# Performance work log

Measured on AMD Instinct MI355X. Metric: run time of the kernel, lower is better.

The kernel has to match this reference:

```python
import jax, jax.numpy as jnp
import numpy as np

N = 100000
E = 3200000


def setup_inputs() -> dict:
    key = jax.random.key(0)
    ks = jax.random.split(key, 12)
    x = jax.random.normal(ks[0], (N, 124), dtype=jnp.float32)
    pos = jax.random.normal(ks[1], (N, 3), dtype=jnp.float32)
    z = jax.random.normal(ks[2], (N,), dtype=jnp.float32)
    edge_index = jax.random.randint(ks[3], (2, E), 0, N, dtype=jnp.int64)
    def lin(k, fin, fout):
        kw, kb = jax.random.split(k)
        s = 1.0 / np.sqrt(fin)
        W = jax.random.uniform(kw, (fin, fout), minval=-s, maxval=s, dtype=jnp.float32)
        b = jax.random.uniform(kb, (fout,), minval=-s, maxval=s, dtype=jnp.float32)
        return W, b
    W1, b1 = lin(ks[4], 128, 256)
    W2, b2 = lin(ks[5], 256, 256)
    W3, b3 = lin(ks[6], 256, 256)
    W4, b4 = lin(ks[7], 256, 1)
    return {"x": x, "pos": pos, "z": z, "edge_index": edge_index,
            "W1": W1, "b1": b1, "W2": W2, "b2": b2,
            "W3": W3, "b3": b3, "W4": W4, "b4": b4}


def reference(x, pos, z, edge_index, W1, b1, W2, b2, W3, b3, W4, b4):
    # features = hstack(x, pos, z[:, None])  -> [N, input_dim]
    feats = jnp.concatenate([x, pos, z[:, None]], axis=1)
    src, dst = edge_index[0], edge_index[1]
    # sum of neighbor (dst) features into each src node: O(E) segment-sum
    sums = jax.ops.segment_sum(feats[dst], src, num_segments=feats.shape[0])
    # per-node L2 normalize (matches torch.linalg.norm per row)
    h = sums / jnp.linalg.norm(sums, axis=1, keepdims=True)
    h = jax.nn.relu(h @ W1 + b1)
    h = jax.nn.relu(h @ W2 + b2)
    h = jax.nn.relu(h @ W3 + b3)
    h = h @ W4 + b4            # [N, 1]
    return jnp.mean(h, axis=0)  # [1]
```

## Files before the change

kernel.cpp:

```cpp
#include <hip/hip_runtime.h>
#include <math.h>

#define N_NODES 100000
#define N_EDGES 3200000
#define BSHIFT 6
#define NBUCK 1563
#define NBLK_E 256
#define EPB 12500
#define CAP 3072
#define BM 96
#define MLP_BLOCKS ((N_NODES + BM - 1) / BM)

typedef _Float16 half8 __attribute__((ext_vector_type(8)));
typedef float f32x4 __attribute__((ext_vector_type(4)));
typedef float f32x2 __attribute__((ext_vector_type(2)));

__device__ __forceinline__ void gload16(const void* gsrc, void* ldst) {
    __builtin_amdgcn_global_load_lds(
        (const __attribute__((address_space(1))) unsigned int*)gsrc,
        (__attribute__((address_space(3))) unsigned int*)ldst,
        16, 0, 0);
}

__global__ __launch_bounds__(256) void prep_kernel(
    const float* __restrict__ x, const float* __restrict__ pos,
    const float* __restrict__ z, unsigned int* __restrict__ feats8,
    const float* __restrict__ W1, _Float16* __restrict__ WT1,
    const float* __restrict__ W2, _Float16* __restrict__ WT2,
    const float* __restrict__ W3, _Float16* __restrict__ WT3)
{
    int idx = blockIdx.x * 256 + threadIdx.x;
    if (idx < N_NODES * 32) {
        int n = idx >> 5, j = idx & 31;
        float v[4];
        #pragma unroll
        for (int k = 0; k < 4; ++k) {
            int f = j * 4 + k;
            if (f < 124)      v[k] = x[n * 124 + f];
            else if (f < 127) v[k] = pos[n * 3 + (f - 124)];
            else              v[k] = z[n];
        }
        int u = 0;
        u = __builtin_amdgcn_cvt_pk_fp8_f32(v[0], v[1], u, false);
        u = __builtin_amdgcn_cvt_pk_fp8_f32(v[2], v[3], u, true);
        feats8[idx] = (unsigned int)u;
        return;
    }
    int i2 = idx - N_NODES * 32;
    if (i2 < 128 * 256) {
        int k = i2 >> 8, c = i2 & 255;
        WT1[c * 128 + k] = (_Float16)W1[i2];
    } else if (i2 < 128 * 256 + 256 * 256) {
        int i = i2 - 128 * 256;
        int k = i >> 8, c = i & 255;
        WT2[c * 256 + k] = (_Float16)W2[i];
    } else if (i2 < 128 * 256 + 2 * 256 * 256) {
        int i = i2 - 128 * 256 - 256 * 256;
        int k = i >> 8, c = i & 255;
        WT3[c * 256 + k] = (_Float16)W3[i];
    }
}

__global__ __launch_bounds__(1024) void coarse_hist_kernel(
    const int* __restrict__ ei, int* __restrict__ gcnt)
{
    __shared__ int bins[NBUCK];
    int t = threadIdx.x, blk = blockIdx.x;
    for (int b = t; b < NBUCK; b += 1024) bins[b] = 0;
    __syncthreads();
    int base = blk * EPB;
    for (int i = t; i < EPB; i += 1024) {
        int src = __builtin_nontemporal_load(&ei[base + i]);
        atomicAdd(&bins[src >> BSHIFT], 1);
    }
    __syncthreads();
    for (int b = t; b < NBUCK; b += 1024)
        gcnt[blk * NBUCK + b] = bins[b];
}

__global__ __launch_bounds__(256) void bucket_tot_kernel(
    const int* __restrict__ gcnt, int* __restrict__ btot)
{
    __shared__ int red[4];
    int b = blockIdx.x, t = threadIdx.x;
    int s = gcnt[t * NBUCK + b];
    #pragma unroll
    for (int off = 32; off > 0; off >>= 1) s += __shfl_xor(s, off, 64);
    if ((t & 63) == 0) red[t >> 6] = s;
    __syncthreads();
    if (t == 0) btot[b] = red[0] + red[1] + red[2] + red[3];
}

__global__ __launch_bounds__(1024) void scan_buckets_kernel(
    const int* __restrict__ btot, int* __restrict__ bbase)
{
    __shared__ int s[1024];
    int t = threadIdx.x;
    int i0 = 2 * t, i1 = 2 * t + 1;
    int v0 = (i0 < NBUCK) ? btot[i0] : 0;
    int v1 = (i1 < NBUCK) ? btot[i1] : 0;
    int sum = v0 + v1;
    s[t] = sum;
    __syncthreads();
    for (int off = 1; off < 1024; off <<= 1) {
        int o = (t >= off) ? s[t - off] : 0;
        __syncthreads();
        s[t] += o;
        __syncthreads();
    }
    int excl = s[t] - sum;
    if (i0 < NBUCK) bbase[i0] = excl;
    if (i1 < NBUCK) bbase[i1] = excl + v0;
    if (i0 == NBUCK - 1) bbase[NBUCK] = excl + v0;
    if (i1 == NBUCK - 1) bbase[NBUCK] = excl + v0 + v1;
}

__global__ __launch_bounds__(256) void colscan_kernel(
    const int* __restrict__ gcnt, const int* __restrict__ bbase,
    int* __restrict__ gbase)
{
    __shared__ int s[NBLK_E];
    int b = blockIdx.x, t = threadIdx.x;
    int v = gcnt[t * NBUCK + b];
    s[t] = v;
    __syncthreads();
    for (int off = 1; off < NBLK_E; off <<= 1) {
        int o = (t >= off) ? s[t - off] : 0;
        __syncthreads();
        s[t] += o;
        __syncthreads();
    }
    gbase[t * NBUCK + b] = bbase[b] + s[t] - v;
}

__global__ __launch_bounds__(1024) void bucket_scatter_kernel(
    const int* __restrict__ ei, const int* __restrict__ gcnt,
    const int* __restrict__ gbase, unsigned int* __restrict__ bucketed)
{
    __shared__ unsigned int val[EPB];
    __shared__ int gd[EPB];
    __shared__ int cur[NBUCK];
    __shared__ int gofs[NBUCK];
    __shared__ int ssum[1024];

    int t = threadIdx.x, blk = blockIdx.x;

    int i0 = 2 * t, i1 = 2 * t + 1;
    int c0 = (i0 < NBUCK) ? gcnt[blk * NBUCK + i0] : 0;
    int c1 = (i1 < NBUCK) ? gcnt[blk * NBUCK + i1] : 0;
    int sum = c0 + c1;
    ssum[t] = sum;
    __syncthreads();
    for (int off = 1; off < 1024; off <<= 1) {
        int o = (t >= off) ? ssum[t - off] : 0;
        __syncthreads();
        ssum[t] += o;
        __syncthreads();
    }
    int excl = ssum[t] - sum;
    if (i0 < NBUCK) { cur[i0] = excl;      gofs[i0] = gbase[blk * NBUCK + i0] - excl; }
    if (i1 < NBUCK) { cur[i1] = excl + c0; gofs[i1] = gbase[blk * NBUCK + i1] - (excl + c0); }
    __syncthreads();

    int base = blk * EPB;
    for (int i = t; i < EPB; i += 1024) {
        int e = base + i;
        int src = __builtin_nontemporal_load(&ei[e]);
        int dst = __builtin_nontemporal_load(&ei[N_EDGES + e]);
        int b = src >> BSHIFT;
        int r = atomicAdd(&cur[b], 1);
        val[r] = (unsigned int)dst | ((unsigned int)(src & 63) << 17);
        gd[r] = gofs[b] + r;
    }
    __syncthreads();

    for (int i = t; i < EPB; i += 1024)
        bucketed[gd[i]] = val[i];
}

__global__ __launch_bounds__(256) void sortagg_kernel(
    const int* __restrict__ bbase, const unsigned int* __restrict__ bucketed,
    const uint2* __restrict__ feats8u2, _Float16* __restrict__ h0)
{
    __shared__ unsigned int srt[CAP];
    __shared__ int excl[64], cur[64];

    int t = threadIdx.x, b = blockIdx.x;
    int segs = bbase[b], cnt = bbase[b + 1] - segs;
    if (cnt > CAP) cnt = CAP;

    if (t < 64) cur[t] = 0;
    __syncthreads();

    for (int i = t; i < cnt; i += 256)
        atomicAdd(&cur[(bucketed[segs + i] >> 17) & 63], 1);
    __syncthreads();

    int v = (t < 64) ? cur[t] : 0;
    if (t < 64) excl[t] = v;
    __syncthreads();
    for (int off = 1; off < 64; off <<= 1) {
        int o = (t >= off && t < 64) ? excl[t - off] : 0;
        __syncthreads();
        if (t < 64) excl[t] += o;
        __syncthreads();
    }
    if (t < 64) { excl[t] -= v; cur[t] = excl[t]; }
    __syncthreads();

    for (int i = t; i < cnt; i += 256) {
        unsigned int p = bucketed[segs + i];
        int r = atomicAdd(&cur[(p >> 17) & 63], 1);
        if (r < CAP) srt[r] = p & 0x1FFFFu;
    }
    __syncthreads();

    int w = t >> 6, lane = t & 63;
    int h = lane >> 4;
    int s = lane & 15;
    const uint2* fb = feats8u2 + s;

#define ACC8(U)                                                     \
    a01 += __builtin_amdgcn_cvt_pk_f32_fp8((U).x, false);           \
    a23 += __builtin_amdgcn_cvt_pk_f32_fp8((U).x, true);            \
    a45 += __builtin_amdgcn_cvt_pk_f32_fp8((U).y, false);           \
    a67 += __builtin_amdgcn_cvt_pk_f32_fp8((U).y, true);

    for (int j = 0; j < 16; ++j) {
        int nl = w * 16 + j;
        int node = b * 64 + nl;
        if (node >= N_NODES) break;
        int start = excl[nl], end = cur[nl];
        f32x2 a01 = {0.f, 0.f}, a23 = {0.f, 0.f};
        f32x2 a45 = {0.f, 0.f}, a67 = {0.f, 0.f};
        int i = start;
        for (; i + 24 <= end; i += 24) {
            uint2 uu[6];
            #pragma unroll
            for (int q = 0; q < 6; ++q)
                uu[q] = fb[(long long)srt[i + 4 * q + h] * 16];
            #pragma unroll
            for (int q = 0; q < 6; ++q) { ACC8(uu[q]); }
        }
        for (; i + 4 <= end; i += 4) {
            uint2 u = fb[(long long)srt[i + h] * 16];
            ACC8(u);
        }
        if (i + h < end) {
            uint2 u = fb[(long long)srt[i + h] * 16];
            ACC8(u);
        }
#define MRG(A)                                                      \
        A[0] += __shfl_xor(A[0], 16, 64);                           \
        A[1] += __shfl_xor(A[1], 16, 64);                           \
        A[0] += __shfl_xor(A[0], 32, 64);                           \
        A[1] += __shfl_xor(A[1], 32, 64);
        MRG(a01) MRG(a23) MRG(a45) MRG(a67)
#undef MRG
        float ss = a01[0]*a01[0] + a01[1]*a01[1] + a23[0]*a23[0] + a23[1]*a23[1]
                 + a45[0]*a45[0] + a45[1]*a45[1] + a67[0]*a67[0] + a67[1]*a67[1];
        #pragma unroll
        for (int off = 8; off > 0; off >>= 1) ss += __shfl_xor(ss, off, 64);
        float inv = 1.0f / sqrtf(ss);
        if (h == 0) {
            union { uint4 u; _Float16 f[8]; } o;
            o.f[0] = (_Float16)(a01[0] * inv); o.f[1] = (_Float16)(a01[1] * inv);
            o.f[2] = (_Float16)(a23[0] * inv); o.f[3] = (_Float16)(a23[1] * inv);
            o.f[4] = (_Float16)(a45[0] * inv); o.f[5] = (_Float16)(a45[1] * inv);
            o.f[6] = (_Float16)(a67[0] * inv); o.f[7] = (_Float16)(a67[1] * inv);
            *reinterpret_cast<uint4*>(&h0[(long long)node * 128 + s * 8]) = o.u;
        }
    }
#undef ACC8
}

__global__ __launch_bounds__(256, 2) void fused_mlp_kernel(
    const _Float16* __restrict__ h0,
    const _Float16* __restrict__ WT1,
    const float* __restrict__ b1,
    const _Float16* __restrict__ WT2,
    const float* __restrict__ b2,
    const _Float16* __restrict__ WT3,
    const float* __restrict__ b3,
    const float* __restrict__ W4,
    float* __restrict__ partials, int M)
{
    __shared__ __align__(16) _Float16 sA[8 * 3072];
    __shared__ __align__(16) _Float16 sB[2][8192];

    const int t = threadIdx.x;
    const int row0 = blockIdx.x * BM;

    const int ap0 = t & 3;
    const int r0 = t >> 2;
    const int ag0 = ap0 ^ ((r0 >> 1) & 3);
    int arow0 = row0 + r0; if (arow0 > M - 1) arow0 = M - 1;
    const _Float16* aSrc0 = h0 + (long long)arow0 * 128 + ag0 * 8;
    const int r1 = (256 + t) >> 2;
    const int ag1 = ap0 ^ ((r1 >> 1) & 3);
    int arow1 = row0 + r1; if (arow1 > M - 1) arow1 = M - 1;
    const _Float16* aSrc1 = h0 + (long long)arow1 * 128 + ag1 * 8;

    const int bc0 = t >> 2;
    const int gb = ap0 ^ ((bc0 >> 1) & 3);

    const int w = t >> 6, lane = t & 63;
    const int wr = w >> 1, wc = w & 1;
    const int lrow = lane & 15, g = lane >> 4;

    unsigned int offA[3], offB[8];
    #pragma unroll
    for (int rt = 0; rt < 3; ++rt) {
        int r = wr * 48 + rt * 16 + lrow;
        offA[rt] = r * 64 + (g ^ ((r >> 1) & 3)) * 16;
    }
    #pragma unroll
    for (int ct = 0; ct < 8; ++ct) {
        int cidx = wc * 128 + ct * 16 + lrow;
        offB[ct] = cidx * 64 + (g ^ ((cidx >> 1) & 3)) * 16;
    }

    float bb1[8], bb2[8], bb3[8], w4v[8];
    #pragma unroll
    for (int ct = 0; ct < 8; ++ct) {
        int col = wc * 128 + ct * 16 + lrow;
        bb1[ct] = b1[col]; bb2[ct] = b2[col];
        bb3[ct] = b3[col]; w4v[ct] = W4[col];
    }

    f32x4 acc[3][8];
    #pragma unroll
    for (int i = 0; i < 3; ++i)
        #pragma unroll
        for (int j = 0; j < 8; ++j)
            acc[i][j] = (f32x4){0.f, 0.f, 0.f, 0.f};

#define STG(WT, Kv, KC, BUF)                                                 \
    {                                                                        \
        _Pragma("unroll")                                                    \
        for (int j = 0; j < 4; ++j)                                          \
            gload16((WT) + (long long)(bc0 + j * 64) * (Kv) + gb * 8 +       \
                        (KC) * 32,                                           \
                    (char*)sB[BUF] + j * 4096 + t * 16);                     \
    }

#define WB(N)                                                                \
    asm volatile("s_waitcnt vmcnt(" #N ")" ::: "memory");                    \
    __builtin_amdgcn_s_barrier();                                            \
    __builtin_amdgcn_sched_barrier(0);

#define EB() __builtin_amdgcn_s_barrier();

#define SEAM()                                                               \
    asm volatile("s_waitcnt lgkmcnt(0)" ::: "memory");                       \
    __builtin_amdgcn_s_barrier();                                            \
    __builtin_amdgcn_sched_barrier(0);

#define STORE_ACTS(BB)                                                       \
    {                                                                        \
        _Pragma("unroll")                                                    \
        for (int ct = 0; ct < 8; ++ct) {                                     \
            int col = wc * 128 + ct * 16 + lrow;                             \
            float bb = (BB)[ct];                                             \
            int chk = col >> 5, kk = col & 31;                               \
            int kg = kk >> 3, ke = kk & 7;                                   \
            _Pragma("unroll")                                                \
            for (int rt = 0; rt < 3; ++rt) {                                 \
                _Pragma("unroll")                                            \
                for (int jj = 0; jj < 4; ++jj) {                             \
                    int rowl = wr * 48 + rt * 16 + g * 4 + jj;               \
                    int slot = kg ^ ((rowl >> 1) & 3);                       \
                    sA[chk * 3072 + rowl * 32 + slot * 8 + ke] =             \
                        (_Float16)fmaxf(acc[rt][ct][jj] + bb, 0.f);          \
                    acc[rt][ct][jj] = 0.f;                                   \
                }                                                            \
            }                                                                \
        }                                                                    \
    }

#define MFMA_CHUNK(KC, BUF)                                                  \
    {                                                                        \
        half8 a[3], bfr[8];                                                  \
        __builtin_amdgcn_s_setprio(1);                                       \
        _Pragma("unroll")                                                    \
        for (int rt = 0; rt < 3; ++rt)                                       \
            a[rt] = *reinterpret_cast<const half8*>(                         \
                (const char*)sA + (KC) * 6144 + offA[rt]);                   \
        _Pragma("unroll")                                                    \
        for (int ct = 0; ct < 8; ++ct)                                       \
            bfr[ct] = *reinterpret_cast<const half8*>(                       \
                (const char*)sB[BUF] + offB[ct]);                            \
        _Pragma("unroll")                                                    \
        for (int rt = 0; rt < 3; ++rt)                                       \
            _Pragma("unroll")                                                \
            for (int ct = 0; ct < 8; ++ct)                                   \
                acc[rt][ct] = __builtin_amdgcn_mfma_f32_16x16x32_f16(        \
                    a[rt], bfr[ct], acc[rt][ct], 0, 0, 0);                   \
        __builtin_amdgcn_s_setprio(0);                                       \
    }

    #pragma unroll
    for (int kc = 0; kc < 4; ++kc) {
        gload16(aSrc0 + kc * 32, (char*)sA + kc * 6144 + t * 16);
        if (t < 128)
            gload16(aSrc1 + kc * 32, (char*)sA + kc * 6144 + 4096 + t * 16);
    }
    STG(WT1, 128, 0, 0)

    STG(WT1, 128, 1, 1)  WB(4)  MFMA_CHUNK(0, 0)  EB()
    STG(WT1, 128, 2, 0)  WB(4)  MFMA_CHUNK(1, 1)  EB()
    STG(WT1, 128, 3, 1)  WB(4)  MFMA_CHUNK(2, 0)  EB()
    STG(WT2, 256, 0, 0)  WB(4)  MFMA_CHUNK(3, 1)  EB()
    STORE_ACTS(bb1) SEAM()
    STG(WT2, 256, 1, 1)  WB(4)  MFMA_CHUNK(0, 0)  EB()
    STG(WT2, 256, 2, 0)  WB(4)  MFMA_CHUNK(1, 1)  EB()
    STG(WT2, 256, 3, 1)  WB(4)  MFMA_CHUNK(2, 0)  EB()
    STG(WT2, 256, 4, 0)  WB(4)  MFMA_CHUNK(3, 1)  EB()
    STG(WT2, 256, 5, 1)  WB(4)  MFMA_CHUNK(4, 0)  EB()
    STG(WT2, 256, 6, 0)  WB(4)  MFMA_CHUNK(5, 1)  EB()
    STG(WT2, 256, 7, 1)  WB(4)  MFMA_CHUNK(6, 0)  EB()
    STG(WT3, 256, 0, 0)  WB(4)  MFMA_CHUNK(7, 1)  EB()
    STORE_ACTS(bb2) SEAM()
    STG(WT3, 256, 1, 1)  WB(4)  MFMA_CHUNK(0, 0)  EB()
    STG(WT3, 256, 2, 0)  WB(4)  MFMA_CHUNK(1, 1)  EB()
    STG(WT3, 256, 3, 1)  WB(4)  MFMA_CHUNK(2, 0)  EB()
    STG(WT3, 256, 4, 0)  WB(4)  MFMA_CHUNK(3, 1)  EB()
    STG(WT3, 256, 5, 1)  WB(4)  MFMA_CHUNK(4, 0)  EB()
    STG(WT3, 256, 6, 0)  WB(4)  MFMA_CHUNK(5, 1)  EB()
    STG(WT3, 256, 7, 1)  WB(4)  MFMA_CHUNK(6, 0)  EB()
                         WB(0)  MFMA_CHUNK(7, 1)  EB()

    float sum = 0.f;
    #pragma unroll
    for (int ct = 0; ct < 8; ++ct) {
        float bb = bb3[ct];
        float w4 = w4v[ct];
        #pragma unroll
        for (int rt = 0; rt < 3; ++rt) {
            #pragma unroll
            for (int jj = 0; jj < 4; ++jj) {
                int row = row0 + wr * 48 + rt * 16 + g * 4 + jj;
                if (row < M) {
                    float vv = fmaxf(acc[rt][ct][jj] + bb, 0.f);
                    sum += vv * w4;
                }
            }
        }
    }
    #pragma unroll
    for (int off = 32; off > 0; off >>= 1) sum += __shfl_xor(sum, off, 64);
    float* redf = reinterpret_cast<float*>(sA);
    if (lane == 0) redf[w] = sum;
    __syncthreads();
    if (t == 0) partials[blockIdx.x] = redf[0] + redf[1] + redf[2] + redf[3];
#undef STG
#undef WB
#undef EB
#undef SEAM
#undef STORE_ACTS
#undef MFMA_CHUNK
}

__global__ __launch_bounds__(256) void final_kernel(
    const float* __restrict__ partials, int n,
    const float* __restrict__ b4, float* __restrict__ out)
{
    __shared__ float buf[256];
    float s = 0.f;
    for (int i = threadIdx.x; i < n; i += 256) s += partials[i];
    buf[threadIdx.x] = s;
    __syncthreads();
    for (int off = 128; off > 0; off >>= 1) {
        if (threadIdx.x < off) buf[threadIdx.x] += buf[threadIdx.x + off];
        __syncthreads();
    }
    if (threadIdx.x == 0) out[0] = buf[0] / (float)N_NODES + b4[0];
}

extern "C" void kernel_launch(void* const* d_in, const int* in_sizes, int n_in,
                              void* d_out, int out_size, void* d_ws, size_t ws_size,
                              hipStream_t stream)
{
    const float* x   = (const float*)d_in[0];
    const float* pos = (const float*)d_in[1];
    const float* z   = (const float*)d_in[2];
    const int*   ei  = (const int*)d_in[3];
    const float* W1  = (const float*)d_in[4];
    const float* b1  = (const float*)d_in[5];
    const float* W2  = (const float*)d_in[6];
    const float* b2  = (const float*)d_in[7];
    const float* W3  = (const float*)d_in[8];
    const float* b3  = (const float*)d_in[9];
    const float* W4  = (const float*)d_in[10];
    const float* b4  = (const float*)d_in[11];
    float* out = (float*)d_out;

    char* ws = (char*)d_ws;
    unsigned int* feats8   = (unsigned int*)(ws);
    _Float16*     h0       = (_Float16*)    (ws + 12800000);
    int*          gcnt     = (int*)         (ws + 38400000);
    int*          gbase    = (int*)         (ws + 40000512);
    int*          btot     = (int*)         (ws + 41601024);
    int*          bbase    = (int*)         (ws + 41607276);
    unsigned int* bucketed = (unsigned int*)(ws + 41613532);
    _Float16*     WT1      = (_Float16*)    (ws + 54413568);
    _Float16*     WT2      = (_Float16*)    (ws + 54479104);
    _Float16*     WT3      = (_Float16*)    (ws + 54610176);
    float*        partials = (float*)       (ws + 54741248);

    {
        int total = N_NODES * 32 + 128 * 256 + 2 * 256 * 256;
        prep_kernel<<<(total + 255) / 256, 256, 0, stream>>>(
            x, pos, z, feats8, W1, WT1, W2, WT2, W3, WT3);
    }

    coarse_hist_kernel<<<NBLK_E, 1024, 0, stream>>>(ei, gcnt);
    bucket_tot_kernel<<<NBUCK, 256, 0, stream>>>(gcnt, btot);
    scan_buckets_kernel<<<1, 1024, 0, stream>>>(btot, bbase);
    colscan_kernel<<<NBUCK, 256, 0, stream>>>(gcnt, bbase, gbase);
    bucket_scatter_kernel<<<NBLK_E, 1024, 0, stream>>>(ei, gcnt, gbase, bucketed);

    sortagg_kernel<<<NBUCK, 256, 0, stream>>>(
        bbase, bucketed, (const uint2*)feats8, h0);

    fused_mlp_kernel<<<MLP_BLOCKS, 256, 0, stream>>>(
        h0, WT1, b1, WT2, b2, WT3, b3, W4, partials, N_NODES);

    final_kernel<<<1, 256, 0, stream>>>(partials, MLP_BLOCKS, b4, out);
}
```

Before: 170.0 us.

## Fuse feature prep into histogram kernel and drop scatter dest LDS array

Merges the fp8 feature packing and weight transpose work into the coarse histogram kernel, so one launch of 256 blocks of 1024 threads does both instead of two separate launches. In the bucket scatter kernel, the per-edge destination array in shared memory is removed. Each element now binary-searches the post-atomic bucket cursors to find its bucket and global offset. This cuts LDS usage (possibly raising occupancy) and one launch, at the cost of about 11 search steps per element and fewer blocks doing the prep work.

After: 177.4 us. 1.04x slower.

```diff
diff --git a/kernel.cpp b/kernel.cpp
--- a/kernel.cpp
+++ b/kernel.cpp
@@ -10,6 +10,8 @@
 #define CAP 3072
 #define BM 96
 #define MLP_BLOCKS ((N_NODES + BM - 1) / BM)
+#define PREP_TOTAL (N_NODES * 32 + 128 * 256 + 2 * 256 * 256)
+#define PREP_PER_BLK ((PREP_TOTAL + NBLK_E - 1) / NBLK_E)
 
 typedef _Float16 half8 __attribute__((ext_vector_type(8)));
 typedef float f32x4 __attribute__((ext_vector_type(4)));
@@ -22,52 +24,53 @@
         16, 0, 0);
 }
 
-__global__ __launch_bounds__(256) void prep_kernel(
+__global__ __launch_bounds__(1024) void prep_hist_kernel(
     const float* __restrict__ x, const float* __restrict__ pos,
     const float* __restrict__ z, unsigned int* __restrict__ feats8,
     const float* __restrict__ W1, _Float16* __restrict__ WT1,
     const float* __restrict__ W2, _Float16* __restrict__ WT2,
-    const float* __restrict__ W3, _Float16* __restrict__ WT3)
-{
-    int idx = blockIdx.x * 256 + threadIdx.x;
-    if (idx < N_NODES * 32) {
-        int n = idx >> 5, j = idx & 31;
-        float v[4];
-        #pragma unroll
-        for (int k = 0; k < 4; ++k) {
-            int f = j * 4 + k;
-            if (f < 124)      v[k] = x[n * 124 + f];
-            else if (f < 127) v[k] = pos[n * 3 + (f - 124)];
-            else              v[k] = z[n];
-        }
-        int u = 0;
-        u = __builtin_amdgcn_cvt_pk_fp8_f32(v[0], v[1], u, false);
-        u = __builtin_amdgcn_cvt_pk_fp8_f32(v[2], v[3], u, true);
-        feats8[idx] = (unsigned int)u;
-        return;
-    }
-    int i2 = idx - N_NODES * 32;
-    if (i2 < 128 * 256) {
-        int k = i2 >> 8, c = i2 & 255;
-        WT1[c * 128 + k] = (_Float16)W1[i2];
-    } else if (i2 < 128 * 256 + 256 * 256) {
-        int i = i2 - 128 * 256;
-        int k = i >> 8, c = i & 255;
-        WT2[c * 256 + k] = (_Float16)W2[i];
-    } else if (i2 < 128 * 256 + 2 * 256 * 256) {
-        int i = i2 - 128 * 256 - 256 * 256;
-        int k = i >> 8, c = i & 255;
-        WT3[c * 256 + k] = (_Float16)W3[i];
-    }
-}
-
-__global__ __launch_bounds__(1024) void coarse_hist_kernel(
+    const float* __restrict__ W3, _Float16* __restrict__ WT3,
     const int* __restrict__ ei, int* __restrict__ gcnt)
 {
     __shared__ int bins[NBUCK];
     int t = threadIdx.x, blk = blockIdx.x;
     for (int b = t; b < NBUCK; b += 1024) bins[b] = 0;
     __syncthreads();
+
+    int pend = blk * PREP_PER_BLK + PREP_PER_BLK;
+    if (pend > PREP_TOTAL) pend = PREP_TOTAL;
+    for (int idx = blk * PREP_PER_BLK + t; idx < pend; idx += 1024) {
+        if (idx < N_NODES * 32) {
+            int n = idx >> 5, j = idx & 31;
+            float v[4];
+            #pragma unroll
+            for (int k = 0; k < 4; ++k) {
+                int f = j * 4 + k;
+                if (f < 124)      v[k] = x[n * 124 + f];
+                else if (f < 127) v[k] = pos[n * 3 + (f - 124)];
+                else              v[k] = z[n];
+            }
+            int u = 0;
+            u = __builtin_amdgcn_cvt_pk_fp8_f32(v[0], v[1], u, false);
+            u = __builtin_amdgcn_cvt_pk_fp8_f32(v[2], v[3], u, true);
+            feats8[idx] = (unsigned int)u;
+        } else {
+            int i2 = idx - N_NODES * 32;
+            if (i2 < 128 * 256) {
+                int k = i2 >> 8, c = i2 & 255;
+                WT1[c * 128 + k] = (_Float16)W1[i2];
+            } else if (i2 < 128 * 256 + 256 * 256) {
+                int i = i2 - 128 * 256;
+                int k = i >> 8, c = i & 255;
+                WT2[c * 256 + k] = (_Float16)W2[i];
+            } else {
+                int i = i2 - 128 * 256 - 256 * 256;
+                int k = i >> 8, c = i & 255;
+                WT3[c * 256 + k] = (_Float16)W3[i];
+            }
+        }
+    }
+
     int base = blk * EPB;
     for (int i = t; i < EPB; i += 1024) {
         int src = __builtin_nontemporal_load(&ei[base + i]);
@@ -138,7 +141,6 @@
     const int* __restrict__ gbase, unsigned int* __restrict__ bucketed)
 {
     __shared__ unsigned int val[EPB];
-    __shared__ int gd[EPB];
     __shared__ int cur[NBUCK];
     __shared__ int gofs[NBUCK];
     __shared__ int ssum[1024];
@@ -170,12 +172,17 @@
         int b = src >> BSHIFT;
         int r = atomicAdd(&cur[b], 1);
         val[r] = (unsigned int)dst | ((unsigned int)(src & 63) << 17);
-        gd[r] = gofs[b] + r;
-    }
-    __syncthreads();
-
-    for (int i = t; i < EPB; i += 1024)
-        bucketed[gd[i]] = val[i];
+    }
+    __syncthreads();
+
+    for (int i = t; i < EPB; i += 1024) {
+        int lo = 0, hi = NBUCK - 1;
+        while (lo < hi) {
+            int mid = (lo + hi) >> 1;
+            if (cur[mid] > i) hi = mid; else lo = mid + 1;
+        }
+        bucketed[gofs[lo] + i] = val[i];
+    }
 }
 
 __global__ __launch_bounds__(256) void sortagg_kernel(
@@ -508,16 +515,13 @@
     _Float16*     WT3      = (_Float16*)    (ws + 54610176);
     float*        partials = (float*)       (ws + 54741248);
 
-    {
-        int total = N_NODES * 32 + 128 * 256 + 2 * 256 * 256;
-        prep_kernel<<<(total + 255) / 256, 256, 0, stream>>>(
-            x, pos, z, feats8, W1, WT1, W2, WT2, W3, WT3);
-    }
-
-    coarse_hist_kernel<<<NBLK_E, 1024, 0, stream>>>(ei, gcnt);
+    prep_hist_kernel<<<NBLK_E, 1024, 0, stream>>>(
+        x, pos, z, feats8, W1, WT1, W2, WT2, W3, WT3, ei, gcnt);
+
     bucket_tot_kernel<<<NBUCK, 256, 0, stream>>>(gcnt, btot);
     scan_buckets_kernel<<<1, 1024, 0, stream>>>(btot, bbase);
     colscan_kernel<<<NBUCK, 256, 0, stream>>>(gcnt, bbase, gbase);
+
     bucket_scatter_kernel<<<NBLK_E, 1024, 0, stream>>>(ei, gcnt, gbase, bucketed);
 
     sortagg_kernel<<<NBUCK, 256, 0, stream>>>(
```
